# Kernel optimization log

Hardware: AMD Instinct MI355X
Metric: run time of the kernel (lower is better)

## Reference

```python
import jax, jax.numpy as jnp
import numpy as np

N, F, H, K, T, O = 4096, 64, 64, 2, 5, 32  # nodes, in_feat, hidden, heads, temporal_steps, out


def setup_inputs() -> dict:
    key = jax.random.key(0)
    ks = jax.random.split(key, 12)
    s = 0.05
    return {
        "node_features": jax.random.normal(ks[0], (N, F), jnp.float32),
        "adj_matrix": jax.random.randint(ks[1], (N, N), 0, 2, jnp.int32),
        "temporal_features": jax.random.normal(ks[2], (N, T, H), jnp.float32),
        # GAT params (stacked over K heads). Linear W: Wh = h @ W.T, so W_gat[k] is [H, F].
        "W_gat": jax.random.normal(ks[3], (K, H, F), jnp.float32) * s,
        "a_src": jax.random.normal(ks[4], (K, H), jnp.float32) * s,  # first half of a (repeat -> column/neighbor index)
        "a_dst": jax.random.normal(ks[5], (K, H), jnp.float32) * s,  # second half of a (repeat_interleave -> row/self index)
        # LSTM (1 layer, input K*H, hidden H), PyTorch gate order i,f,g,o
        "W_ih": jax.random.normal(ks[6], (4 * H, K * H), jnp.float32) * s,
        "W_hh": jax.random.normal(ks[7], (4 * H, H), jnp.float32) * s,
        "b_ih": jax.random.normal(ks[8], (4 * H,), jnp.float32) * s,
        "b_hh": jax.random.normal(ks[9], (4 * H,), jnp.float32) * s,
        # fc
        "fc_W": jax.random.normal(ks[10], (O, H), jnp.float32) * s,
        "fc_b": jax.random.normal(ks[11], (O,), jnp.float32) * s,
    }


def reference(node_features, adj_matrix, temporal_features,
              W_gat, a_src, a_dst, W_ih, W_hh, b_ih, b_hh, fc_W, fc_b):
    # ---- GAT heads (vectorized over K) ----
    Wh = jnp.einsum("nf,khf->knh", node_features, W_gat)          # [K,N,H]
    # a([Wh_i, Wh_j]) == a_src.Wh_j + a_dst.Wh_i; e[p,q] = lrelu(dst[p] + src[q])
    s_src = jnp.einsum("knh,kh->kn", Wh, a_src)                    # column term
    s_dst = jnp.einsum("knh,kh->kn", Wh, a_dst)                    # row term
    e = jax.nn.leaky_relu(s_dst[:, :, None] + s_src[:, None, :], 0.2)  # [K,N,N]
    e = jnp.where(adj_matrix[None, :, :] > 0, e, jnp.float32(-1e9))
    att = jax.nn.softmax(e, axis=-1)                               # dropout = identity (eval)
    h_prime = jax.nn.elu(jnp.einsum("kpq,kqh->kph", att, Wh))      # [K,N,H]
    h = jnp.transpose(h_prime, (1, 0, 2)).reshape(N, K * H)        # concat heads [N, K*H]
    # ---- LSTM over seq of length 1 (h.unsqueeze(1)); h0 = c0 = 0 ----
    gates = h @ W_ih.T + b_ih + b_hh                               # h0 @ W_hh.T == 0
    i, f, g, o = jnp.split(gates, 4, axis=-1)
    c = jax.nn.sigmoid(i) * jnp.tanh(g)                            # f * c0 == 0
    h_t = jax.nn.sigmoid(o) * jnp.tanh(c)                          # [N,H]
    return h_t @ fc_W.T + fc_b                                     # [N,O]
```

## Files before the change

kernel.cpp:

```cpp
#include <hip/hip_runtime.h>


#define NN 4096

typedef __attribute__((ext_vector_type(8))) short bf16x8;
typedef __attribute__((ext_vector_type(4))) float f32x4;

__device__ inline unsigned short bf_rne(float f) {
    unsigned u = __float_as_uint(f);
    u += 0x7fffu + ((u >> 16) & 1u);
    return (unsigned short)(u >> 16);
}

__device__ inline float sigf(float x) { return 1.f / (1.f + __expf(-x)); }

__global__ __launch_bounds__(256) void convert_w(
    const float* __restrict__ W_ih, const float* __restrict__ b_ih,
    const float* __restrict__ b_hh, const float* __restrict__ fc_W,
    unsigned short* __restrict__ Wpk, unsigned short* __restrict__ fcb,
    float* __restrict__ biasg)
{
    const int idx = blockIdx.x * 256 + threadIdx.x;
    if (idx < 24576) {
        const int j = idx & 7, lane = (idx >> 3) & 63;
        const int k0 = (idx >> 9) & 3, t = idx >> 11;
        const int jj = t * 16 + (lane & 15);
        const int m = k0 * 32 + (lane >> 4) * 8 + j;
        const int sr = (jj < 64) ? jj : 64 + jj;
        Wpk[idx] = bf_rne(W_ih[sr * 128 + m]);
    } else if (idx < 26624) {
        const int o = idx - 24576;
        const int j = o & 7, lane = (o >> 3) & 63;
        const int k0 = (o >> 9) & 1, t = o >> 10;
        const int row = t * 16 + (lane & 15);
        const int m = k0 * 32 + (lane >> 4) * 8 + j;
        fcb[o] = bf_rne(fc_W[row * 64 + m]);
    } else if (idx < 26816) {
        const int j = idx - 26624;
        const int sr = (j < 64) ? j : 64 + j;
        biasg[j] = b_ih[sr] + b_hh[sr];
    }
}

__global__ __launch_bounds__(256) void gat_prep(
    const float* __restrict__ X, const float* __restrict__ Wg,
    const float* __restrict__ a_src, const float* __restrict__ a_dst,
    unsigned short* __restrict__ whB, float* __restrict__ ssrc,
    float* __restrict__ sdst)
{
    __shared__ float X_lds[64][64];
    __shared__ float Wh_lds[64][65];
    __shared__ float spart[64][4][2];
    const int t = threadIdx.x;
    const int n0 = blockIdx.x * 64;
#pragma unroll
    for (int i = 0; i < 16; ++i) {
        int idx = t + i * 256;
        X_lds[idx >> 6][idx & 63] = X[n0 * 64 + idx];
    }
    __syncthreads();
    const int h = t & 63, rg = t >> 6;
    for (int k = 0; k < 2; ++k) {
        float acc[16];
#pragma unroll
        for (int r = 0; r < 16; ++r) acc[r] = 0.f;
        for (int f0 = 0; f0 < 64; f0 += 4) {
            const float4 w4 = *(const float4*)&Wg[(k * 64 + h) * 64 + f0];
#pragma unroll
            for (int r = 0; r < 16; ++r) {
                const float4 x4 = *(const float4*)&X_lds[rg * 16 + r][f0];
                acc[r] += w4.x * x4.x + w4.y * x4.y + w4.z * x4.z + w4.w * x4.w;
            }
        }
        if (k) __syncthreads();
#pragma unroll
        for (int r = 0; r < 16; ++r) Wh_lds[rg * 16 + r][h] = acc[r];
        __syncthreads();
        {
            const int r = t & 63, qa = t >> 6;
            float ps = 0.f, pd = 0.f;
#pragma unroll
            for (int i = 0; i < 16; ++i) {
                const int hh = qa * 16 + i;
                const float v = Wh_lds[r][hh];
                ps += v * a_src[k * 64 + hh];
                pd += v * a_dst[k * 64 + hh];
            }
            spart[r][qa][0] = ps;
            spart[r][qa][1] = pd;
        }
        {
#pragma unroll
            for (int pid = t; pid < 512; pid += 256) {
                const int n = pid & 15, qg = (pid >> 4) & 3;
                const int qb_loc = (pid >> 6) & 1, f = pid >> 7;
                const int qb = (n0 >> 5) + qb_loc;
                unsigned pk[4];
#pragma unroll
                for (int i = 0; i < 4; ++i) {
                    const int r = qb_loc * 32 + qg * 8 + 2 * i;
                    unsigned lo = bf_rne(Wh_lds[r][f * 16 + n]);
                    unsigned hi = bf_rne(Wh_lds[r + 1][f * 16 + n]);
                    pk[i] = lo | (hi << 16);
                }
                uint4* dst = (uint4*)&whB[(((k * 4 + f) * 128 + qb) * 512) + (qg * 16 + n) * 8];
                *dst = make_uint4(pk[0], pk[1], pk[2], pk[3]);
            }
        }
        __syncthreads();
        if (t < 64) {
            float s0 = spart[t][0][0] + spart[t][1][0] + spart[t][2][0] + spart[t][3][0];
            float s1 = spart[t][0][1] + spart[t][1][1] + spart[t][2][1] + spart[t][3][1];
            ssrc[k * NN + n0 + t] = s0;
            sdst[k * NN + n0 + t] = s1;
        }
    }
}

__global__ __launch_bounds__(1024) void gat_attn(
    const int* __restrict__ adj, const unsigned short* __restrict__ whB,
    const float* __restrict__ ssrc, const float* __restrict__ sdst,
    const unsigned short* __restrict__ Wpk, const unsigned short* __restrict__ fcb,
    const float* __restrict__ biasg, const float* __restrict__ fc_b,
    float* __restrict__ out)
{
    __shared__ float S_all[16][2][16][64];
    __shared__ float z_all[16][2][16];
    __shared__ unsigned long long bits_lds[16][65];
    unsigned short* h_lds = (unsigned short*)&S_all[0][0][0][0];
    float* gate_lds = (float*)((char*)&S_all[0][0][0][0] + 4608);

    const int tid = threadIdx.x;
    const int wave = tid >> 6, lane = tid & 63;
    const int rloc = lane & 15, qg = lane >> 4;
    const int p0 = blockIdx.x * 16;
    const int p = p0 + rloc;

    {
        const int* __restrict__ arow = adj + (long)(p0 + wave) * NN;
        unsigned long long myw = 0ull;
#pragma unroll 8
        for (int it = 0; it < 64; ++it) {
            const int v = arow[it * 64 + lane];
            const unsigned long long bal = __ballot(v != 0);
            if (lane == it) myw = bal;
        }
        bits_lds[wave][lane] = myw;
    }
    __syncthreads();

    const float sd0 = sdst[p], sd1 = sdst[NN + p];
    const unsigned short* __restrict__ whB_l = whB + lane * 8;

    f32x4 acc[2][4];
#pragma unroll
    for (int k = 0; k < 2; ++k)
#pragma unroll
        for (int f = 0; f < 4; ++f)
            acc[k][f] = (f32x4){0.f, 0.f, 0.f, 0.f};
    float z0 = 0.f, z1 = 0.f;

    const int qbase = wave * 256;
    for (int chunk = 0; chunk < 4; ++chunk) {
        const unsigned long long bw = bits_lds[rloc][wave * 4 + chunk];
#pragma unroll
        for (int kk = 0; kk < 2; ++kk) {
            const int q0 = qbase + chunk * 64 + kk * 32 + qg * 8;
            const int qb = wave * 8 + chunk * 2 + kk;
            const unsigned byte8 = ((unsigned)(bw >> (kk * 32)) >> (qg * 8)) & 0xffu;
            const float4 sa0 = *(const float4*)(ssrc + q0);
            const float4 sa1 = *(const float4*)(ssrc + q0 + 4);
            const float4 sb0 = *(const float4*)(ssrc + NN + q0);
            const float4 sb1 = *(const float4*)(ssrc + NN + q0 + 4);
            const float s0v[8] = {sa0.x, sa0.y, sa0.z, sa0.w, sa1.x, sa1.y, sa1.z, sa1.w};
            const float s1v[8] = {sb0.x, sb0.y, sb0.z, sb0.w, sb1.x, sb1.y, sb1.z, sb1.w};
            union { bf16x8 v; unsigned short u[8]; } fa0, fa1;
#pragma unroll
            for (int j = 0; j < 8; ++j) {
                const bool on = (byte8 & (1u << j)) != 0u;
                float e0 = sd0 + s0v[j];
                e0 = fmaxf(e0, 0.2f * e0);
                const float w0 = on ? __expf(e0) : 0.f;
                z0 += w0;
                fa0.u[j] = bf_rne(w0);
                float e1 = sd1 + s1v[j];
                e1 = fmaxf(e1, 0.2f * e1);
                const float w1 = on ? __expf(e1) : 0.f;
                z1 += w1;
                fa1.u[j] = bf_rne(w1);
            }
#pragma unroll
            for (int f = 0; f < 4; ++f) {
                const bf16x8 b0 = *(const bf16x8*)(whB_l + ((f * 128 + qb) << 9));
                acc[0][f] = __builtin_amdgcn_mfma_f32_16x16x32_bf16(fa0.v, b0, acc[0][f], 0, 0, 0);
                const bf16x8 b1 = *(const bf16x8*)(whB_l + (((4 + f) * 128 + qb) << 9));
                acc[1][f] = __builtin_amdgcn_mfma_f32_16x16x32_bf16(fa1.v, b1, acc[1][f], 0, 0, 0);
            }
        }
    }
    z0 += __shfl_xor(z0, 16); z0 += __shfl_xor(z0, 32);
    z1 += __shfl_xor(z1, 16); z1 += __shfl_xor(z1, 32);
    if (lane < 16) { z_all[wave][0][lane] = z0; z_all[wave][1][lane] = z1; }
#pragma unroll
    for (int k = 0; k < 2; ++k)
#pragma unroll
        for (int f = 0; f < 4; ++f)
#pragma unroll
            for (int j = 0; j < 4; ++j)
                S_all[wave][k][qg * 4 + j][f * 16 + rloc] = acc[k][f][j];
    __syncthreads();
    float vreg[2]; int vk[2], vr[2], vh[2];
#pragma unroll
    for (int i = 0; i < 2; ++i) {
        const int idx = tid + i * 1024;
        const int k = idx >> 10, rr = (idx >> 6) & 15, hh = idx & 63;
        float s = 0.f, z = 0.f;
#pragma unroll
        for (int w = 0; w < 16; ++w) {
            s += S_all[w][k][rr][hh];
            z += z_all[w][k][rr];
        }
        float v = s / z;
        vreg[i] = v > 0.f ? v : expm1f(v);
        vk[i] = k; vr[i] = rr; vh[i] = hh;
    }
    __syncthreads();
#pragma unroll
    for (int i = 0; i < 2; ++i)
        h_lds[vr[i] * 136 + vk[i] * 64 + vh[i]] = bf_rne(vreg[i]);
    __syncthreads();

    const int c = lane & 15, g4 = lane >> 4;
    if (wave < 12) {
        const int t = wave;
        f32x4 ga = (f32x4){0.f, 0.f, 0.f, 0.f};
#pragma unroll
        for (int k0 = 0; k0 < 4; ++k0) {
            const bf16x8 a = *(const bf16x8*)&h_lds[c * 136 + k0 * 32 + g4 * 8];
            const bf16x8 b = *(const bf16x8*)&Wpk[((t * 4 + k0) * 64 + lane) * 8];
            ga = __builtin_amdgcn_mfma_f32_16x16x32_bf16(a, b, ga, 0, 0, 0);
        }
        const float bb = biasg[t * 16 + c];
#pragma unroll
        for (int j = 0; j < 4; ++j)
            gate_lds[(t >> 2) * 1088 + (g4 * 4 + j) * 68 + (t & 3) * 16 + c] = ga[j] + bb;
    }
    __syncthreads();
    if (tid < 1024) {
        const int n = tid >> 6, hh = tid & 63;
        const float iv = gate_lds[n * 68 + hh];
        const float gv = gate_lds[1088 + n * 68 + hh];
        const float ov = gate_lds[2176 + n * 68 + hh];
        const float cv = sigf(iv) * tanhf(gv);
        const float htv = sigf(ov) * tanhf(cv);
        h_lds[n * 136 + hh] = bf_rne(htv);
    }
    __syncthreads();
    if (wave < 2) {
        const int t2 = wave;
        f32x4 fa = (f32x4){0.f, 0.f, 0.f, 0.f};
#pragma unroll
        for (int k0 = 0; k0 < 2; ++k0) {
            const bf16x8 a = *(const bf16x8*)&h_lds[c * 136 + k0 * 32 + g4 * 8];
            const bf16x8 b = *(const bf16x8*)&fcb[((t2 * 2 + k0) * 64 + lane) * 8];
            fa = __builtin_amdgcn_mfma_f32_16x16x32_bf16(a, b, fa, 0, 0, 0);
        }
        const float fb = fc_b[t2 * 16 + c];
#pragma unroll
        for (int j = 0; j < 4; ++j)
            out[(p0 + g4 * 4 + j) * 32 + t2 * 16 + c] = fa[j] + fb;
    }
}

extern "C" void kernel_launch(void* const* d_in, const int* in_sizes, int n_in,
                              void* d_out, int out_size, void* d_ws, size_t ws_size,
                              hipStream_t stream) {
    const float* X     = (const float*)d_in[0];
    const int*   adj   = (const int*)d_in[1];
    const float* Wg    = (const float*)d_in[3];
    const float* a_src = (const float*)d_in[4];
    const float* a_dst = (const float*)d_in[5];
    const float* W_ih  = (const float*)d_in[6];
    const float* b_ih  = (const float*)d_in[8];
    const float* b_hh  = (const float*)d_in[9];
    const float* fc_W  = (const float*)d_in[10];
    const float* fc_b  = (const float*)d_in[11];
    float* out = (float*)d_out;

    char* ws = (char*)d_ws;
    unsigned short* whB = (unsigned short*)ws;
    float* ssrc = (float*)(ws + (1 << 20));
    float* sdst = (float*)(ws + (1 << 20) + (32 << 10));
    char* ws2 = ws + (1 << 20) + (64 << 10);
    unsigned short* Wpk = (unsigned short*)ws2;
    unsigned short* fcb = (unsigned short*)(ws2 + (48 << 10));
    float* biasg = (float*)(ws2 + (52 << 10));

    hipLaunchKernelGGL(convert_w, dim3(105), dim3(256), 0, stream,
                       W_ih, b_ih, b_hh, fc_W, Wpk, fcb, biasg);
    hipLaunchKernelGGL(gat_prep, dim3(64), dim3(256), 0, stream,
                       X, Wg, a_src, a_dst, whB, ssrc, sdst);
    hipLaunchKernelGGL(gat_attn, dim3(256), dim3(1024), 0, stream,
                       adj, whB, ssrc, sdst, Wpk, fcb, biasg, fc_b, out);
}
```

Baseline: 62.51 us.

## Merge prep kernels, move adjacency bit-packing to prep, factor exp out of attention

Merges convert_w and gat_prep into one launch, and adds blocks to it that bit-pack the 64MB int adjacency matrix into a bitmask in global memory. The attention kernel then loads the precomputed bits instead of scanning adjacency itself. Per-element exp is replaced by products of precomputed exp(s) and exp(0.2s) per node, using exp(a+b)=exp(a)exp(b) with the leaky-relu branch chosen by comparing the product to 1. The code also uses a packed bf16 convert instruction. This removes transcendental work from the inner loop and one kernel launch, at the cost of an extra bitmask round trip through global memory and possible overflow in the exp products.

New measurement: 68.87 us. 1.1x slower.

```diff
diff --git a/kernel.cpp b/kernel.cpp
--- a/kernel.cpp
+++ b/kernel.cpp
@@ -12,47 +12,69 @@
     return (unsigned short)(u >> 16);
 }
 
+__device__ inline unsigned cvt_pk_bf16(float lo, float hi) {
+    unsigned r;
+    asm("v_cvt_pk_bf16_f32 %0, %1, %2" : "=v"(r) : "v"(lo), "v"(hi));
+    return r;
+}
+
 __device__ inline float sigf(float x) { return 1.f / (1.f + __expf(-x)); }
 
-__global__ __launch_bounds__(256) void convert_w(
-    const float* __restrict__ W_ih, const float* __restrict__ b_ih,
-    const float* __restrict__ b_hh, const float* __restrict__ fc_W,
+__global__ __launch_bounds__(256) void prep_all(
+    const float* __restrict__ X, const float* __restrict__ Wg,
+    const float* __restrict__ a_src, const float* __restrict__ a_dst,
+    const int* __restrict__ adj, const float* __restrict__ W_ih,
+    const float* __restrict__ b_ih, const float* __restrict__ b_hh,
+    const float* __restrict__ fc_W,
+    unsigned short* __restrict__ whB, float* __restrict__ e1s,
+    float* __restrict__ e2s, float* __restrict__ e1d, float* __restrict__ e2d,
+    unsigned long long* __restrict__ adjbits,
     unsigned short* __restrict__ Wpk, unsigned short* __restrict__ fcb,
     float* __restrict__ biasg)
-{
-    const int idx = blockIdx.x * 256 + threadIdx.x;
-    if (idx < 24576) {
-        const int j = idx & 7, lane = (idx >> 3) & 63;
-        const int k0 = (idx >> 9) & 3, t = idx >> 11;
-        const int jj = t * 16 + (lane & 15);
-        const int m = k0 * 32 + (lane >> 4) * 8 + j;
-        const int sr = (jj < 64) ? jj : 64 + jj;
-        Wpk[idx] = bf_rne(W_ih[sr * 128 + m]);
-    } else if (idx < 26624) {
-        const int o = idx - 24576;
-        const int j = o & 7, lane = (o >> 3) & 63;
-        const int k0 = (o >> 9) & 1, t = o >> 10;
-        const int row = t * 16 + (lane & 15);
-        const int m = k0 * 32 + (lane >> 4) * 8 + j;
-        fcb[o] = bf_rne(fc_W[row * 64 + m]);
-    } else if (idx < 26816) {
-        const int j = idx - 26624;
-        const int sr = (j < 64) ? j : 64 + j;
-        biasg[j] = b_ih[sr] + b_hh[sr];
-    }
-}
-
-__global__ __launch_bounds__(256) void gat_prep(
-    const float* __restrict__ X, const float* __restrict__ Wg,
-    const float* __restrict__ a_src, const float* __restrict__ a_dst,
-    unsigned short* __restrict__ whB, float* __restrict__ ssrc,
-    float* __restrict__ sdst)
 {
     __shared__ float X_lds[64][64];
     __shared__ float Wh_lds[64][65];
     __shared__ float spart[64][4][2];
     const int t = threadIdx.x;
-    const int n0 = blockIdx.x * 64;
+    const int bid = blockIdx.x;
+
+    if (bid >= 169) {
+        const int wave = t >> 6, lane = t & 63;
+        const long wid = (long)(bid - 169) * 4 + wave;
+#pragma unroll 4
+        for (int it = 0; it < 64; ++it) {
+            const long w = wid * 64 + it;
+            const int v = adj[w * 64 + lane];
+            const unsigned long long b = __ballot(v != 0);
+            if (lane == 0) adjbits[w] = b;
+        }
+        return;
+    }
+    if (bid >= 64) {
+        const int idx = (bid - 64) * 256 + t;
+        if (idx < 24576) {
+            const int j = idx & 7, lane = (idx >> 3) & 63;
+            const int k0 = (idx >> 9) & 3, tt = idx >> 11;
+            const int jj = tt * 16 + (lane & 15);
+            const int m = k0 * 32 + (lane >> 4) * 8 + j;
+            const int sr = (jj < 64) ? jj : 64 + jj;
+            Wpk[idx] = bf_rne(W_ih[sr * 128 + m]);
+        } else if (idx < 26624) {
+            const int o = idx - 24576;
+            const int j = o & 7, lane = (o >> 3) & 63;
+            const int k0 = (o >> 9) & 1, tt = o >> 10;
+            const int row = tt * 16 + (lane & 15);
+            const int m = k0 * 32 + (lane >> 4) * 8 + j;
+            fcb[o] = bf_rne(fc_W[row * 64 + m]);
+        } else if (idx < 26816) {
+            const int j = idx - 26624;
+            const int sr = (j < 64) ? j : 64 + j;
+            biasg[j] = b_ih[sr] + b_hh[sr];
+        }
+        return;
+    }
+
+    const int n0 = bid * 64;
 #pragma unroll
     for (int i = 0; i < 16; ++i) {
         int idx = t + i * 256;
@@ -111,15 +133,19 @@
         if (t < 64) {
             float s0 = spart[t][0][0] + spart[t][1][0] + spart[t][2][0] + spart[t][3][0];
             float s1 = spart[t][0][1] + spart[t][1][1] + spart[t][2][1] + spart[t][3][1];
-            ssrc[k * NN + n0 + t] = s0;
-            sdst[k * NN + n0 + t] = s1;
+            e1s[k * NN + n0 + t] = __expf(s0);
+            e2s[k * NN + n0 + t] = __expf(0.2f * s0);
+            e1d[k * NN + n0 + t] = __expf(s1);
+            e2d[k * NN + n0 + t] = __expf(0.2f * s1);
         }
     }
 }
 
 __global__ __launch_bounds__(1024) void gat_attn(
-    const int* __restrict__ adj, const unsigned short* __restrict__ whB,
-    const float* __restrict__ ssrc, const float* __restrict__ sdst,
+    const unsigned long long* __restrict__ adjbits,
+    const unsigned short* __restrict__ whB,
+    const float* __restrict__ e1s, const float* __restrict__ e2s,
+    const float* __restrict__ e1d, const float* __restrict__ e2d,
     const unsigned short* __restrict__ Wpk, const unsigned short* __restrict__ fcb,
     const float* __restrict__ biasg, const float* __restrict__ fc_b,
     float* __restrict__ out)
@@ -136,20 +162,11 @@
     const int p0 = blockIdx.x * 16;
     const int p = p0 + rloc;
 
-    {
-        const int* __restrict__ arow = adj + (long)(p0 + wave) * NN;
-        unsigned long long myw = 0ull;
-#pragma unroll 8
-        for (int it = 0; it < 64; ++it) {
-            const int v = arow[it * 64 + lane];
-            const unsigned long long bal = __ballot(v != 0);
-            if (lane == it) myw = bal;
-        }
-        bits_lds[wave][lane] = myw;
-    }
-    __syncthreads();
-
-    const float sd0 = sdst[p], sd1 = sdst[NN + p];
+    bits_lds[tid >> 6][tid & 63] = adjbits[(long)(p0 + (tid >> 6)) * 64 + (tid & 63)];
+    __syncthreads();
+
+    const float e1p0 = e1d[p], e2p0 = e2d[p];
+    const float e1p1 = e1d[NN + p], e2p1 = e2d[NN + p];
     const unsigned short* __restrict__ whB_l = whB + lane * 8;
 
     f32x4 acc[2][4];
@@ -168,26 +185,38 @@
             const int q0 = qbase + chunk * 64 + kk * 32 + qg * 8;
             const int qb = wave * 8 + chunk * 2 + kk;
             const unsigned byte8 = ((unsigned)(bw >> (kk * 32)) >> (qg * 8)) & 0xffu;
-            const float4 sa0 = *(const float4*)(ssrc + q0);
-            const float4 sa1 = *(const float4*)(ssrc + q0 + 4);
-            const float4 sb0 = *(const float4*)(ssrc + NN + q0);
-            const float4 sb1 = *(const float4*)(ssrc + NN + q0 + 4);
-            const float s0v[8] = {sa0.x, sa0.y, sa0.z, sa0.w, sa1.x, sa1.y, sa1.z, sa1.w};
-            const float s1v[8] = {sb0.x, sb0.y, sb0.z, sb0.w, sb1.x, sb1.y, sb1.z, sb1.w};
-            union { bf16x8 v; unsigned short u[8]; } fa0, fa1;
+            const float4 qa0 = *(const float4*)(e1s + q0);
+            const float4 qa1 = *(const float4*)(e1s + q0 + 4);
+            const float4 qb0 = *(const float4*)(e2s + q0);
+            const float4 qb1 = *(const float4*)(e2s + q0 + 4);
+            const float4 qc0 = *(const float4*)(e1s + NN + q0);
+            const float4 qc1 = *(const float4*)(e1s + NN + q0 + 4);
+            const float4 qd0 = *(const float4*)(e2s + NN + q0);
+            const float4 qd1 = *(const float4*)(e2s + NN + q0 + 4);
+            const float q1v0[8] = {qa0.x, qa0.y, qa0.z, qa0.w, qa1.x, qa1.y, qa1.z, qa1.w};
+            const float q2v0[8] = {qb0.x, qb0.y, qb0.z, qb0.w, qb1.x, qb1.y, qb1.z, qb1.w};
+            const float q1v1[8] = {qc0.x, qc0.y, qc0.z, qc0.w, qc1.x, qc1.y, qc1.z, qc1.w};
+            const float q2v1[8] = {qd0.x, qd0.y, qd0.z, qd0.w, qd1.x, qd1.y, qd1.z, qd1.w};
+            float w0a[8], w1a[8];
 #pragma unroll
             for (int j = 0; j < 8; ++j) {
                 const bool on = (byte8 & (1u << j)) != 0u;
-                float e0 = sd0 + s0v[j];
-                e0 = fmaxf(e0, 0.2f * e0);
-                const float w0 = on ? __expf(e0) : 0.f;
+                const float pp0 = e1p0 * q1v0[j];
+                float w0 = pp0 > 1.f ? pp0 : e2p0 * q2v0[j];
+                w0 = on ? w0 : 0.f;
                 z0 += w0;
-                fa0.u[j] = bf_rne(w0);
-                float e1 = sd1 + s1v[j];
-                e1 = fmaxf(e1, 0.2f * e1);
-                const float w1 = on ? __expf(e1) : 0.f;
+                w0a[j] = w0;
+                const float pp1 = e1p1 * q1v1[j];
+                float w1 = pp1 > 1.f ? pp1 : e2p1 * q2v1[j];
+                w1 = on ? w1 : 0.f;
                 z1 += w1;
-                fa1.u[j] = bf_rne(w1);
+                w1a[j] = w1;
+            }
+            union { bf16x8 v; unsigned w[4]; } fa0, fa1;
+#pragma unroll
+            for (int i = 0; i < 4; ++i) {
+                fa0.w[i] = cvt_pk_bf16(w0a[2 * i], w0a[2 * i + 1]);
+                fa1.w[i] = cvt_pk_bf16(w1a[2 * i], w1a[2 * i + 1]);
             }
 #pragma unroll
             for (int f = 0; f < 4; ++f) {
@@ -246,13 +275,14 @@
             gate_lds[(t >> 2) * 1088 + (g4 * 4 + j) * 68 + (t & 3) * 16 + c] = ga[j] + bb;
     }
     __syncthreads();
-    if (tid < 1024) {
+    {
         const int n = tid >> 6, hh = tid & 63;
         const float iv = gate_lds[n * 68 + hh];
         const float gv = gate_lds[1088 + n * 68 + hh];
         const float ov = gate_lds[2176 + n * 68 + hh];
         const float cv = sigf(iv) * tanhf(gv);
         const float htv = sigf(ov) * tanhf(cv);
+        __syncthreads();
         h_lds[n * 136 + hh] = bf_rne(htv);
     }
     __syncthreads();
@@ -289,17 +319,19 @@
 
     char* ws = (char*)d_ws;
     unsigned short* whB = (unsigned short*)ws;
-    float* ssrc = (float*)(ws + (1 << 20));
-    float* sdst = (float*)(ws + (1 << 20) + (32 << 10));
-    char* ws2 = ws + (1 << 20) + (64 << 10);
+    float* e1s = (float*)(ws + (1 << 20));
+    float* e2s = (float*)(ws + (1 << 20) + (32 << 10));
+    float* e1d = (float*)(ws + (1 << 20) + (64 << 10));
+    float* e2d = (float*)(ws + (1 << 20) + (96 << 10));
+    unsigned long long* adjbits = (unsigned long long*)(ws + (1 << 20) + (128 << 10));
+    char* ws2 = ws + (3 << 20) + (128 << 10);
     unsigned short* Wpk = (unsigned short*)ws2;
     unsigned short* fcb = (unsigned short*)(ws2 + (48 << 10));
     float* biasg = (float*)(ws2 + (52 << 10));
 
-    hipLaunchKernelGGL(convert_w, dim3(105), dim3(256), 0, stream,
-                       W_ih, b_ih, b_hh, fc_W, Wpk, fcb, biasg);
-    hipLaunchKernelGGL(gat_prep, dim3(64), dim3(256), 0, stream,
-                       X, Wg, a_src, a_dst, whB, ssrc, sdst);
+    hipLaunchKernelGGL(prep_all, dim3(1193), dim3(256), 0, stream,
+                       X, Wg, a_src, a_dst, adj, W_ih, b_ih, b_hh, fc_W,
+                       whB, e1s, e2s, e1d, e2d, adjbits, Wpk, fcb, biasg);
     hipLaunchKernelGGL(gat_attn, dim3(256), dim3(1024), 0, stream,
-                       adj, whB, ssrc, sdst, Wpk, fcb, biasg, fc_b, out);
-}
+                       adjbits, whB, e1s, e2s, e1d, e2d, Wpk, fcb, biasg, fc_b, out);
+}
```
